# Optimization experiments

Hardware: AMD Instinct MI355X
Metric: run time of the kernel (lower is better)

Reference implementation:

```python
import jax, jax.numpy as jnp
import numpy as np

N_ITER = 4  # n_iter
NEG = -1e9  # masked-score fill (softmax-safe stand-in for -inf)


def _mfvi(x, mask, ternary, global_):
    """MFVI message passing between head (H) and node (Z) variables with global nodes.

    x:       [B, L, D] unary scores for Z nodes
    mask:    [B, L]    padding mask (nonzero = valid token)
    ternary: [D, D, H] ternary factor scores f(Z_i=a, Z_j=b, H-channel c)
    global_: [G, D, H] global-node factor scores
    Defaults: norm=softmax, regularize=1, stepsize=1, damping=0, async_update,
    no tensor decomposition, mode='all-attn', block_msg=False, output_prob=False.
    """
    B, L, D = x.shape
    m1 = (mask != 0)                                             # [B, L]
    pair_valid = m1[:, None, :, None] & m1[:, None, None, :]     # [B, 1, L, L]
    unary = x                                                    # pos_embed='none'
    Qz = jax.nn.softmax(unary, axis=-1)                          # [B, L, D]
    F_Z = unary
    neg = jnp.asarray(NEG, x.dtype)
    for _ in range(N_ITER):
        # --- H update: scores for head variable H_{i,c} over candidate heads j ---
        # F_Hs[n,h,i,j] = sum_{a,b} Qz[n,i,a] * ternary[a,b,h] * Qz[n,j,b]
        F_Hs = jnp.einsum('nia,abh,njb->nhij', Qz, ternary, Qz)  # [B, H, L, L]
        F_Hs = jnp.where(pair_valid, F_Hs, neg)
        # global-node columns: F_Hg[n,h,i,g] = sum_a Qz[n,i,a] * global_[g,a,h]
        F_Hg = jnp.einsum('nia,gah->nhig', Qz, global_)          # [B, H, L, G]
        F_H = jnp.concatenate([F_Hs, F_Hg], axis=-1)             # [B, H, L, L+G]
        Q_H = jax.nn.softmax(F_H, axis=-1)                       # regularize_H = 1
        Qhs, Qhg = Q_H[..., :L], Q_H[..., L:]
        # --- Z update (async: uses fresh Q_H) ---
        # message to Z_i from its chosen head j
        msg_i = jnp.einsum('nhij,njb,abh->nia', Qhs, Qz, ternary)
        # message to Z_j from dependents i (block_msg=False keeps it)
        msg_j = jnp.einsum('nhij,nia,abh->njb', Qhs, Qz, ternary)
        # message to Z_i from global nodes
        msg_g = jnp.einsum('nhig,gah->nia', Qhg, global_)
        F_Z = unary + msg_i + msg_j + msg_g                      # [B, L, D]
        Qz = jax.nn.softmax(F_Z, axis=-1)                        # regularize_Z = 1
    # output_prob=False -> unnormalized scores, zeroed at padding
    return jnp.where(m1[..., None], F_Z, jnp.zeros_like(F_Z))


def setup_inputs() -> dict:
    key = jax.random.key(0)
    k1, k2, k3 = jax.random.split(key, 3)
    B, L, D, H, G = 4, 1024, 128, 8, 64
    x = jax.random.normal(k1, (B, L, D), dtype=jnp.float32)
    mask = jnp.ones((B, L), dtype=jnp.int32)
    ternary = jax.random.normal(k2, (D, D, H), dtype=jnp.float32)          # init std=1
    global_ = jax.random.normal(k3, (G, D, H), dtype=jnp.float32) / np.sqrt(D)
    return {"x": x, "mask": mask, "ternary": ternary, "global_": global_}


def reference(x, mask, ternary, global_):
    return _mfvi(x, mask, ternary, global_)
```

## Files before the change

### kernel.cpp

```cpp
#include <hip/hip_runtime.h>
#include <math.h>

#define Bn 4
#define Ln 1024
#define Dn 128
#define Hn 8
#define Gn 64
#define NITERS 4

typedef _Float16 f16;
typedef _Float16 half8 __attribute__((ext_vector_type(8)));
typedef _Float16 half4v __attribute__((ext_vector_type(4)));
typedef float floatx4 __attribute__((ext_vector_type(4)));

#define WPAD 136
#define PPAD 72

#define MFMA(a, b, c) __builtin_amdgcn_mfma_f32_16x16x32_f16((a), (b), (c), 0, 0, 0)

__device__ __forceinline__ void gl_lds16(const f16* g, f16* l) {
    __builtin_amdgcn_global_load_lds(
        (const __attribute__((address_space(1))) void*)(g),
        (__attribute__((address_space(3))) void*)(l),
        16, 0, 0);
}

__device__ __forceinline__ void issue_tiles(const f16* us, const f16* ub, int sb,
                                            f16* UsB, f16* UbB, int w, int l) {
    #pragma unroll
    for (int k = 0; k < 4; k++) {
        int c = w * 4 + k;
        {
            int r = c * 4 + (l >> 4); int g = (l & 15) ^ (r & 7);
            gl_lds16(us + (size_t)r * Dn + g * 8, UsB + c * 512);
        }
        {
            int r = c * 8 + (l >> 3); int g = (l & 7) ^ (r & 7);
            gl_lds16(ub + (size_t)r * sb + g * 8, UbB + c * 512);
        }
    }
}

__global__ void repack_kernel(const float* __restrict__ ter, const float* __restrict__ glb,
                              f16* __restrict__ TpA, f16* __restrict__ TpB,
                              f16* __restrict__ GpA, f16* __restrict__ Gpt) {
    int idx = blockIdx.x * 256 + threadIdx.x;
    if (idx < Dn * Dn * Hn) {
        int h = idx % Hn; int b = (idx / Hn) % Dn; int a = idx / (Hn * Dn);
        f16 v = (f16)ter[idx];
        TpA[((size_t)h * Dn + a) * Dn + b] = v;
        TpB[((size_t)h * Dn + b) * Dn + a] = v;
    }
    if (idx < Gn * Dn * Hn) {
        int h = idx % Hn; int a = (idx / Hn) % Dn; int g = idx / (Hn * Dn);
        f16 v = (f16)glb[idx];
        GpA[((size_t)h * Gn + g) * Dn + a] = v;
        Gpt[((size_t)h * Dn + a) * Gn + g] = v;
    }
}

__global__ void softmax_rows_kernel(const float* __restrict__ in, f16* __restrict__ out) {
    int row = blockIdx.x;
    int t = threadIdx.x;
    __shared__ float red[2];
    float v = in[(size_t)row * Dn + t];
    float m = v;
    #pragma unroll
    for (int off = 1; off < 64; off <<= 1) m = fmaxf(m, __shfl_xor(m, off, 64));
    if ((t & 63) == 0) red[t >> 6] = m;
    __syncthreads();
    m = fmaxf(red[0], red[1]);
    float e = __expf(v - m);
    float s = e;
    #pragma unroll
    for (int off = 1; off < 64; off <<= 1) s += __shfl_xor(s, off, 64);
    __syncthreads();
    if ((t & 63) == 0) red[t >> 6] = s;
    __syncthreads();
    s = red[0] + red[1];
    out[(size_t)row * Dn + t] = (f16)(e / s);
}

__launch_bounds__(256, 4)
__global__ void uv_kernel(const f16* __restrict__ Qz, const f16* __restrict__ TpA,
                          const f16* __restrict__ TpB,
                          f16* __restrict__ U, f16* __restrict__ Ut, f16* __restrict__ Vt) {
    int bx = blockIdx.x;
    int h  = blockIdx.y;
    int n  = blockIdx.z;
    int t  = threadIdx.x;
    int w = t >> 6, l = t & 63, m = l & 15, q = l >> 4;

    __shared__ __align__(16) f16 Ts[128 * WPAD];

    int jrow = bx * 64 + w * 16 + m;
    const f16* qbase = Qz + ((size_t)n * Ln + jrow) * Dn;
    half8 aq[4];
    #pragma unroll
    for (int ks = 0; ks < 4; ks++)
        aq[ks] = *(const half8*)(qbase + ks * 32 + q * 8);

    size_t hoff = (size_t)(n * Hn + h);
    int jr0 = bx * 64 + w * 16 + 4 * q;

    {
        const f16* src = TpA + (size_t)h * Dn * Dn;
        for (int ii = 0; ii < 8; ii++) {
            int idx = t + 256 * ii; int r = idx >> 4, c = idx & 15;
            *(float4*)&Ts[r * WPAD + c * 8] = *(const float4*)(src + (size_t)r * Dn + c * 8);
        }
        __syncthreads();
        #pragma unroll
        for (int ct = 0; ct < 8; ct++) {
            floatx4 acc = {0.f, 0.f, 0.f, 0.f};
            #pragma unroll
            for (int ks = 0; ks < 4; ks++) {
                half8 b = *(const half8*)&Ts[(ct * 16 + m) * WPAD + ks * 32 + q * 8];
                acc = MFMA(aq[ks], b, acc);
            }
            f16* ub = U + (hoff * Ln + jr0) * Dn + ct * 16 + m;
            #pragma unroll
            for (int reg = 0; reg < 4; reg++) ub[(size_t)reg * Dn] = (f16)acc[reg];
            half4v pk = { (f16)acc[0], (f16)acc[1], (f16)acc[2], (f16)acc[3] };
            *(half4v*)(Ut + (hoff * Dn + ct * 16 + m) * Ln + jr0) = pk;
        }
        __syncthreads();
    }
    {
        const f16* src = TpB + (size_t)h * Dn * Dn;
        for (int ii = 0; ii < 8; ii++) {
            int idx = t + 256 * ii; int r = idx >> 4, c = idx & 15;
            *(float4*)&Ts[r * WPAD + c * 8] = *(const float4*)(src + (size_t)r * Dn + c * 8);
        }
        __syncthreads();
        #pragma unroll
        for (int ct = 0; ct < 8; ct++) {
            floatx4 acc = {0.f, 0.f, 0.f, 0.f};
            #pragma unroll
            for (int ks = 0; ks < 4; ks++) {
                half8 b = *(const half8*)&Ts[(ct * 16 + m) * WPAD + ks * 32 + q * 8];
                acc = MFMA(aq[ks], b, acc);
            }
            half4v pk = { (f16)acc[0], (f16)acc[1], (f16)acc[2], (f16)acc[3] };
            *(half4v*)(Vt + (hoff * Dn + ct * 16 + m) * Ln + jr0) = pk;
        }
    }
}

__launch_bounds__(256, 2)
__global__ void msgi_kernel(const f16* __restrict__ Qz, const f16* __restrict__ U,
                            const f16* __restrict__ Ut, const f16* __restrict__ GpA,
                            const f16* __restrict__ Gpt, const int* __restrict__ mask,
                            f16* __restrict__ Macc, float* __restrict__ rowLinv) {
    int p = blockIdx.x;
    int h  = p & 7;
    int it = (p >> 3) & 15;
    int n  = p >> 7;
    int t = threadIdx.x;
    int w = t >> 6, l = t & 63, m = l & 15, q = l >> 4;
    int rh = w >> 1, ch = w & 1;
    int ih = w >> 1, ah = w & 1;

    __shared__ __align__(16) f16 Us[2][64 * 128];
    __shared__ __align__(16) f16 Ub[2][128 * 64];
    __shared__ __align__(16) f16 Ps[64 * PPAD];
    __shared__ int jms[2][64];
    __shared__ float lpart[2][64];
    __shared__ float linvS[64];

    half8 bq[2][4];
    #pragma unroll
    for (int ib = 0; ib < 2; ib++) {
        const f16* qr = Qz + ((size_t)n * Ln + it * 64 + ch * 32 + ib * 16 + m) * Dn;
        #pragma unroll
        for (int ks = 0; ks < 4; ks++)
            bq[ib][ks] = *(const half8*)(qr + ks * 32 + q * 8);
    }
    int im[2];
    #pragma unroll
    for (int ib = 0; ib < 2; ib++)
        im[ib] = mask[n * Ln + it * 64 + ch * 32 + ib * 16 + m];

    float lacc[2] = {0.f, 0.f};
    floatx4 Oacc[2][4];
    #pragma unroll
    for (int ib = 0; ib < 2; ib++)
        #pragma unroll
        for (int at = 0; at < 4; at++) Oacc[ib][at] = (floatx4){0.f, 0.f, 0.f, 0.f};

    size_t hoff = (size_t)(n * Hn + h);

    issue_tiles(U + hoff * Ln * Dn, Ut + hoff * Dn * Ln, Ln, Us[0], Ub[0], w, l);
    if (t < 64) jms[0][t] = mask[n * Ln + t];
    __syncthreads();

    for (int jt = 0; jt < 17; jt++) {
        int cur = jt & 1, nxt = cur ^ 1;
        if (jt + 1 < 17) {
            const f16 *us, *ub; int sb;
            if (jt + 1 < 16) {
                us = U + (hoff * Ln + (size_t)(jt + 1) * 64) * Dn;
                ub = Ut + hoff * Dn * Ln + (jt + 1) * 64;
                sb = Ln;
            } else {
                us = GpA + (size_t)h * Gn * Dn;
                ub = Gpt + (size_t)h * Dn * Gn;
                sb = Gn;
            }
            issue_tiles(us, ub, sb, Us[nxt], Ub[nxt], w, l);
            if (t < 64) jms[nxt][t] = (jt + 1 < 16) ? mask[n * Ln + (jt + 1) * 64 + t] : 1;
        }
        int isg = (jt == 16);
        #pragma unroll
        for (int jb = 0; jb < 2; jb++) {
            int r0 = rh * 32 + jb * 16 + m;
            half8 au[4];
            #pragma unroll
            for (int ks = 0; ks < 4; ks++)
                au[ks] = *(const half8*)&Us[cur][((size_t)r0 << 7) + ((((ks << 2) + q)) ^ (r0 & 7)) * 8];
            int jmr[4];
            #pragma unroll
            for (int reg = 0; reg < 4; reg++)
                jmr[reg] = jms[cur][rh * 32 + jb * 16 + 4 * q + reg];
            #pragma unroll
            for (int ib = 0; ib < 2; ib++) {
                floatx4 s = {0.f, 0.f, 0.f, 0.f};
                #pragma unroll
                for (int ks = 0; ks < 4; ks++) s = MFMA(au[ks], bq[ib][ks], s);
                half4v pk;
                #pragma unroll
                for (int reg = 0; reg < 4; reg++) {
                    float p2 = (isg || (im[ib] && jmr[reg])) ? __expf(fminf(s[reg], 11.f)) : 0.f;
                    lacc[ib] += p2;
                    pk[reg] = (f16)p2;
                }
                *(half4v*)&Ps[(ch * 32 + ib * 16 + m) * PPAD + rh * 32 + jb * 16 + 4 * q] = pk;
            }
        }
        __syncthreads();

        #pragma unroll
        for (int kst = 0; kst < 2; kst++) {
            half8 aP[2];
            #pragma unroll
            for (int ib = 0; ib < 2; ib++)
                aP[ib] = *(const half8*)&Ps[(ih * 32 + ib * 16 + m) * PPAD + kst * 32 + q * 8];
            #pragma unroll
            for (int at = 0; at < 4; at++) {
                int r0 = ah * 64 + at * 16 + m;
                half8 bU = *(const half8*)&Ub[cur][((size_t)r0 << 6) + ((((kst << 2) + q)) ^ (r0 & 7)) * 8];
                #pragma unroll
                for (int ib = 0; ib < 2; ib++)
                    Oacc[ib][at] = MFMA(aP[ib], bU, Oacc[ib][at]);
            }
        }
        __syncthreads();
    }

    #pragma unroll
    for (int ib = 0; ib < 2; ib++) {
        float v = lacc[ib];
        v += __shfl_xor(v, 16, 64);
        v += __shfl_xor(v, 32, 64);
        lacc[ib] = v;
    }
    if (q == 0) {
        lpart[rh][ch * 32 + m] = lacc[0];
        lpart[rh][ch * 32 + 16 + m] = lacc[1];
    }
    __syncthreads();
    size_t rbase = hoff * Ln + (size_t)it * 64;
    if (t < 64) {
        float inv = 1.0f / (lpart[0][t] + lpart[1][t]);
        linvS[t] = inv;
        int mk = mask[n * Ln + it * 64 + t];
        rowLinv[rbase + t] = mk ? inv : 0.f;
    }
    __syncthreads();
    f16* Mo = Macc + rbase * Dn;
    #pragma unroll
    for (int ib = 0; ib < 2; ib++)
        #pragma unroll
        for (int reg = 0; reg < 4; reg++) {
            int row = ih * 32 + ib * 16 + 4 * q + reg;
            float inv = linvS[row];
            #pragma unroll
            for (int at = 0; at < 4; at++)
                Mo[(size_t)row * Dn + ah * 64 + at * 16 + m] = (f16)(Oacc[ib][at][reg] * inv);
        }
}

__launch_bounds__(256, 2)
__global__ void msgj_kernel(const f16* __restrict__ Qz, const f16* __restrict__ U,
                            const f16* __restrict__ Vt, const int* __restrict__ mask,
                            const float* __restrict__ rowLinv, f16* __restrict__ Macc) {
    int p = blockIdx.x;
    int h  = p & 7;
    int jt = (p >> 3) & 15;
    int n  = p >> 7;
    int t = threadIdx.x;
    int w = t >> 6, l = t & 63, m = l & 15, q = l >> 4;
    int ihs = w >> 1, jhs = w & 1;
    int jh2 = w >> 1, bh = w & 1;

    __shared__ __align__(16) f16 Qs[2][64 * 128];
    __shared__ __align__(16) f16 Vb[2][128 * 64];
    __shared__ __align__(16) f16 Psj[64 * PPAD];
    __shared__ float lvS[2][64];

    size_t hoff = (size_t)(n * Hn + h);

    half8 bu[2][4];
    #pragma unroll
    for (int jb = 0; jb < 2; jb++) {
        const f16* ur = U + (hoff * Ln + (size_t)jt * 64 + jhs * 32 + jb * 16 + m) * Dn;
        #pragma unroll
        for (int ks = 0; ks < 4; ks++)
            bu[jb][ks] = *(const half8*)(ur + ks * 32 + q * 8);
    }
    int jm[2];
    #pragma unroll
    for (int jb = 0; jb < 2; jb++)
        jm[jb] = mask[n * Ln + jt * 64 + jhs * 32 + jb * 16 + m];

    floatx4 Oacc[2][4];
    #pragma unroll
    for (int jb = 0; jb < 2; jb++)
        #pragma unroll
        for (int bt = 0; bt < 4; bt++) Oacc[jb][bt] = (floatx4){0.f, 0.f, 0.f, 0.f};

    issue_tiles(Qz + (size_t)n * Ln * Dn, Vt + hoff * Dn * Ln, Ln, Qs[0], Vb[0], w, l);
    if (t < 64) lvS[0][t] = rowLinv[hoff * Ln + t];
    __syncthreads();

    for (int it2 = 0; it2 < 16; it2++) {
        int cur = it2 & 1, nxt = cur ^ 1;
        if (it2 + 1 < 16) {
            issue_tiles(Qz + ((size_t)n * Ln + (size_t)(it2 + 1) * 64) * Dn,
                        Vt + hoff * Dn * Ln + (it2 + 1) * 64, Ln, Qs[nxt], Vb[nxt], w, l);
            if (t < 64) lvS[nxt][t] = rowLinv[hoff * Ln + (it2 + 1) * 64 + t];
        }
        #pragma unroll
        for (int ib = 0; ib < 2; ib++) {
            int r0 = ihs * 32 + ib * 16 + m;
            half8 aq2[4];
            #pragma unroll
            for (int ks = 0; ks < 4; ks++)
                aq2[ks] = *(const half8*)&Qs[cur][((size_t)r0 << 7) + ((((ks << 2) + q)) ^ (r0 & 7)) * 8];
            float lv[4];
            #pragma unroll
            for (int reg = 0; reg < 4; reg++)
                lv[reg] = lvS[cur][ihs * 32 + ib * 16 + 4 * q + reg];
            #pragma unroll
            for (int jb = 0; jb < 2; jb++) {
                floatx4 s = {0.f, 0.f, 0.f, 0.f};
                #pragma unroll
                for (int ks = 0; ks < 4; ks++) s = MFMA(aq2[ks], bu[jb][ks], s);
                half4v pk;
                #pragma unroll
                for (int reg = 0; reg < 4; reg++) {
                    float p2 = jm[jb] ? __expf(fminf(s[reg], 11.f)) * lv[reg] : 0.f;
                    pk[reg] = (f16)p2;
                }
                *(half4v*)&Psj[(jhs * 32 + jb * 16 + m) * PPAD + ihs * 32 + ib * 16 + 4 * q] = pk;
            }
        }
        __syncthreads();

        #pragma unroll
        for (int kst = 0; kst < 2; kst++) {
            half8 aP[2];
            #pragma unroll
            for (int jb = 0; jb < 2; jb++)
                aP[jb] = *(const half8*)&Psj[(jh2 * 32 + jb * 16 + m) * PPAD + kst * 32 + q * 8];
            #pragma unroll
            for (int bt = 0; bt < 4; bt++) {
                int r0 = bh * 64 + bt * 16 + m;
                half8 bV = *(const half8*)&Vb[cur][((size_t)r0 << 6) + ((((kst << 2) + q)) ^ (r0 & 7)) * 8];
                #pragma unroll
                for (int jb = 0; jb < 2; jb++)
                    Oacc[jb][bt] = MFMA(aP[jb], bV, Oacc[jb][bt]);
            }
        }
        __syncthreads();
    }

    f16* Mo = Macc + (hoff * Ln + (size_t)jt * 64) * Dn;
    #pragma unroll
    for (int jb = 0; jb < 2; jb++)
        #pragma unroll
        for (int reg = 0; reg < 4; reg++) {
            int row = jh2 * 32 + jb * 16 + 4 * q + reg;
            #pragma unroll
            for (int bt = 0; bt < 4; bt++) {
                f16* p2 = &Mo[(size_t)row * Dn + bh * 64 + bt * 16 + m];
                *p2 = (f16)((float)*p2 + Oacc[jb][bt][reg]);
            }
        }
}

__global__ void combine_kernel(const float* __restrict__ x, const f16* __restrict__ Macc,
                               const int* __restrict__ mask, float* __restrict__ out,
                               f16* __restrict__ Qzh, int do_softmax, int do_mask) {
    int row = blockIdx.x;
    int t = threadIdx.x;
    __shared__ float red[2];
    int n = row >> 10;
    float acc = x[(size_t)row * Dn + t];
    const f16* mp = Macc + (size_t)n * Hn * Ln * Dn + (size_t)(row & 1023) * Dn + t;
    #pragma unroll
    for (int h = 0; h < Hn; h++) acc += (float)mp[(size_t)h * Ln * Dn];
    float o = acc;
    if (do_mask && mask[row] == 0) o = 0.f;
    out[(size_t)row * Dn + t] = o;
    if (do_softmax) {
        float m = acc;
        #pragma unroll
        for (int off = 1; off < 64; off <<= 1) m = fmaxf(m, __shfl_xor(m, off, 64));
        if ((t & 63) == 0) red[t >> 6] = m;
        __syncthreads();
        m = fmaxf(red[0], red[1]);
        float e = __expf(acc - m);
        float s = e;
        #pragma unroll
        for (int off = 1; off < 64; off <<= 1) s += __shfl_xor(s, off, 64);
        __syncthreads();
        if ((t & 63) == 0) red[t >> 6] = s;
        __syncthreads();
        s = red[0] + red[1];
        Qzh[(size_t)row * Dn + t] = (f16)(e / s);
    }
}

extern "C" void kernel_launch(void* const* d_in, const int* in_sizes, int n_in,
                              void* d_out, int out_size, void* d_ws, size_t ws_size,
                              hipStream_t stream) {
    const float* x       = (const float*)d_in[0];
    const int*   mask    = (const int*)d_in[1];
    const float* ternary = (const float*)d_in[2];
    const float* global_ = (const float*)d_in[3];
    float* out = (float*)d_out;
    (void)ws_size; (void)n_in; (void)in_sizes; (void)out_size;

    char* ws = (char*)d_ws;
    size_t o = 0;
    f16* Qzh = (f16*)(ws + o); o += (size_t)Bn * Ln * Dn * 2;
    f16* U   = (f16*)(ws + o); o += (size_t)Bn * Hn * Ln * Dn * 2;
    f16* Ut  = (f16*)(ws + o); o += (size_t)Bn * Hn * Ln * Dn * 2;
    f16* Vt  = (f16*)(ws + o); o += (size_t)Bn * Hn * Ln * Dn * 2;
    f16* TpA = (f16*)(ws + o); o += (size_t)Hn * Dn * Dn * 2;
    f16* TpB = (f16*)(ws + o); o += (size_t)Hn * Dn * Dn * 2;
    f16* GpA = (f16*)(ws + o); o += (size_t)Hn * Gn * Dn * 2;
    f16* Gpt = (f16*)(ws + o); o += (size_t)Hn * Dn * Gn * 2;
    float* rowLinv = (float*)(ws + o); o += (size_t)Bn * Hn * Ln * 4;
    f16* Macc = (f16*)(ws + o); o += (size_t)Bn * Hn * Ln * Dn * 2;

    repack_kernel<<<(Dn * Dn * Hn + 255) / 256, 256, 0, stream>>>(ternary, global_, TpA, TpB, GpA, Gpt);
    softmax_rows_kernel<<<Bn * Ln, 128, 0, stream>>>(x, Qzh);

    for (int it = 0; it < NITERS; it++) {
        uv_kernel<<<dim3(Ln / 64, Hn, Bn), 256, 0, stream>>>(Qzh, TpA, TpB, U, Ut, Vt);
        msgi_kernel<<<dim3(Ln / 64 * Hn * Bn), 256, 0, stream>>>(Qzh, U, Ut, GpA, Gpt, mask, Macc, rowLinv);
        msgj_kernel<<<dim3(Ln / 64 * Hn * Bn), 256, 0, stream>>>(Qzh, U, Vt, mask, rowLinv, Macc);
        combine_kernel<<<Bn * Ln, 128, 0, stream>>>(x, Macc, mask, out, Qzh,
                                                    (it < NITERS - 1) ? 1 : 0,
                                                    (it == NITERS - 1) ? 1 : 0);
    }
}
```

Measured before the change: 384.0 us.

## Keep attention probabilities in registers by permuting Ut/Vt/Gpt column layout

Each wave now computes scores for all 64 key rows of its query half, so the MFMA output fragments can be reassembled directly into the A-operand of the next MFMA without staging P through shared memory. To make the register fragment ordering match the K dimension, the Ut, Vt and Gpt buffers are written with a permuted column order. This removes the Ps/Psj LDS round trip and one barrier per tile, and the row-sum reduction no longer needs cross-wave partials. In exchange, the score MFMAs are duplicated across the two waves that share a query half, which doubles that part of the work.

```diff
diff --git a/kernel.cpp b/kernel.cpp
--- a/kernel.cpp
+++ b/kernel.cpp
@@ -14,9 +14,10 @@
 typedef float floatx4 __attribute__((ext_vector_type(4)));
 
 #define WPAD 136
-#define PPAD 72
 
 #define MFMA(a, b, c) __builtin_amdgcn_mfma_f32_16x16x32_f16((a), (b), (c), 0, 0, 0)
+
+union h8u { half8 h; half4v v[2]; };
 
 __device__ __forceinline__ void gl_lds16(const f16* g, f16* l) {
     __builtin_amdgcn_global_load_lds(
@@ -55,7 +56,8 @@
         int h = idx % Hn; int a = (idx / Hn) % Dn; int g = idx / (Hn * Dn);
         f16 v = (f16)glb[idx];
         GpA[((size_t)h * Gn + g) * Dn + a] = v;
-        Gpt[((size_t)h * Dn + a) * Gn + g] = v;
+        int pos = ((g >> 5) << 5) | (((g >> 2) & 3) << 3) | (((g >> 4) & 1) << 2) | (g & 3);
+        Gpt[((size_t)h * Dn + a) * Gn + pos] = v;
     }
 }
 
@@ -102,6 +104,7 @@
 
     size_t hoff = (size_t)(n * Hn + h);
     int jr0 = bx * 64 + w * 16 + 4 * q;
+    int jrp = bx * 64 + (w >> 1) * 32 + q * 8 + (w & 1) * 4;
 
     {
         const f16* src = TpA + (size_t)h * Dn * Dn;
@@ -122,7 +125,7 @@
             #pragma unroll
             for (int reg = 0; reg < 4; reg++) ub[(size_t)reg * Dn] = (f16)acc[reg];
             half4v pk = { (f16)acc[0], (f16)acc[1], (f16)acc[2], (f16)acc[3] };
-            *(half4v*)(Ut + (hoff * Dn + ct * 16 + m) * Ln + jr0) = pk;
+            *(half4v*)(Ut + (hoff * Dn + ct * 16 + m) * Ln + jrp) = pk;
         }
         __syncthreads();
     }
@@ -142,7 +145,7 @@
                 acc = MFMA(aq[ks], b, acc);
             }
             half4v pk = { (f16)acc[0], (f16)acc[1], (f16)acc[2], (f16)acc[3] };
-            *(half4v*)(Vt + (hoff * Dn + ct * 16 + m) * Ln + jr0) = pk;
+            *(half4v*)(Vt + (hoff * Dn + ct * 16 + m) * Ln + jrp) = pk;
         }
     }
 }
@@ -158,14 +161,12 @@
     int n  = p >> 7;
     int t = threadIdx.x;
     int w = t >> 6, l = t & 63, m = l & 15, q = l >> 4;
-    int rh = w >> 1, ch = w & 1;
-    int ih = w >> 1, ah = w & 1;
+    int ch = w & 1;
+    int ah = w >> 1;
 
     __shared__ __align__(16) f16 Us[2][64 * 128];
     __shared__ __align__(16) f16 Ub[2][128 * 64];
-    __shared__ __align__(16) f16 Ps[64 * PPAD];
-    __shared__ int jms[2][64];
-    __shared__ float lpart[2][64];
+    __shared__ __align__(16) int jms[2][64];
     __shared__ float linvS[64];
 
     half8 bq[2][4];
@@ -211,17 +212,16 @@
             if (t < 64) jms[nxt][t] = (jt + 1 < 16) ? mask[n * Ln + (jt + 1) * 64 + t] : 1;
         }
         int isg = (jt == 16);
-        #pragma unroll
-        for (int jb = 0; jb < 2; jb++) {
-            int r0 = rh * 32 + jb * 16 + m;
+        half4v hv[4][2];
+        #pragma unroll
+        for (int jb = 0; jb < 4; jb++) {
+            int r0 = jb * 16 + m;
             half8 au[4];
             #pragma unroll
             for (int ks = 0; ks < 4; ks++)
                 au[ks] = *(const half8*)&Us[cur][((size_t)r0 << 7) + ((((ks << 2) + q)) ^ (r0 & 7)) * 8];
-            int jmr[4];
-            #pragma unroll
-            for (int reg = 0; reg < 4; reg++)
-                jmr[reg] = jms[cur][rh * 32 + jb * 16 + 4 * q + reg];
+            int4 jmr = *(const int4*)&jms[cur][jb * 16 + 4 * q];
+            int jm4[4] = { jmr.x, jmr.y, jmr.z, jmr.w };
             #pragma unroll
             for (int ib = 0; ib < 2; ib++) {
                 floatx4 s = {0.f, 0.f, 0.f, 0.f};
@@ -230,21 +230,24 @@
                 half4v pk;
                 #pragma unroll
                 for (int reg = 0; reg < 4; reg++) {
-                    float p2 = (isg || (im[ib] && jmr[reg])) ? __expf(fminf(s[reg], 11.f)) : 0.f;
+                    float p2 = (isg || (im[ib] && jm4[reg])) ? __expf(fminf(s[reg], 11.f)) : 0.f;
                     lacc[ib] += p2;
                     pk[reg] = (f16)p2;
                 }
-                *(half4v*)&Ps[(ch * 32 + ib * 16 + m) * PPAD + rh * 32 + jb * 16 + 4 * q] = pk;
-            }
-        }
-        __syncthreads();
+                hv[jb][ib] = pk;
+            }
+        }
 
         #pragma unroll
         for (int kst = 0; kst < 2; kst++) {
             half8 aP[2];
             #pragma unroll
-            for (int ib = 0; ib < 2; ib++)
-                aP[ib] = *(const half8*)&Ps[(ih * 32 + ib * 16 + m) * PPAD + kst * 32 + q * 8];
+            for (int ib = 0; ib < 2; ib++) {
+                h8u u;
+                u.v[0] = hv[2 * kst][ib];
+                u.v[1] = hv[2 * kst + 1][ib];
+                aP[ib] = u.h;
+            }
             #pragma unroll
             for (int at = 0; at < 4; at++) {
                 int r0 = ah * 64 + at * 16 + m;
@@ -264,25 +267,23 @@
         v += __shfl_xor(v, 32, 64);
         lacc[ib] = v;
     }
-    if (q == 0) {
-        lpart[rh][ch * 32 + m] = lacc[0];
-        lpart[rh][ch * 32 + 16 + m] = lacc[1];
+    if (ah == 0 && q == 0) {
+        linvS[ch * 32 + m]      = 1.0f / lacc[0];
+        linvS[ch * 32 + 16 + m] = 1.0f / lacc[1];
     }
     __syncthreads();
     size_t rbase = hoff * Ln + (size_t)it * 64;
     if (t < 64) {
-        float inv = 1.0f / (lpart[0][t] + lpart[1][t]);
-        linvS[t] = inv;
+        float inv = linvS[t];
         int mk = mask[n * Ln + it * 64 + t];
         rowLinv[rbase + t] = mk ? inv : 0.f;
     }
-    __syncthreads();
     f16* Mo = Macc + rbase * Dn;
     #pragma unroll
     for (int ib = 0; ib < 2; ib++)
         #pragma unroll
         for (int reg = 0; reg < 4; reg++) {
-            int row = ih * 32 + ib * 16 + 4 * q + reg;
+            int row = ch * 32 + ib * 16 + 4 * q + reg;
             float inv = linvS[row];
             #pragma unroll
             for (int at = 0; at < 4; at++)
@@ -300,13 +301,12 @@
     int n  = p >> 7;
     int t = threadIdx.x;
     int w = t >> 6, l = t & 63, m = l & 15, q = l >> 4;
-    int ihs = w >> 1, jhs = w & 1;
-    int jh2 = w >> 1, bh = w & 1;
+    int jhs = w & 1;
+    int bh  = w >> 1;
 
     __shared__ __align__(16) f16 Qs[2][64 * 128];
     __shared__ __align__(16) f16 Vb[2][128 * 64];
-    __shared__ __align__(16) f16 Psj[64 * PPAD];
-    __shared__ float lvS[2][64];
+    __shared__ __align__(16) float lvS[2][64];
 
     size_t hoff = (size_t)(n * Hn + h);
 
@@ -340,17 +340,16 @@
                         Vt + hoff * Dn * Ln + (it2 + 1) * 64, Ln, Qs[nxt], Vb[nxt], w, l);
             if (t < 64) lvS[nxt][t] = rowLinv[hoff * Ln + (it2 + 1) * 64 + t];
         }
-        #pragma unroll
-        for (int ib = 0; ib < 2; ib++) {
-            int r0 = ihs * 32 + ib * 16 + m;
+        half4v hv[4][2];
+        #pragma unroll
+        for (int ibt = 0; ibt < 4; ibt++) {
+            int r0 = ibt * 16 + m;
             half8 aq2[4];
             #pragma unroll
             for (int ks = 0; ks < 4; ks++)
                 aq2[ks] = *(const half8*)&Qs[cur][((size_t)r0 << 7) + ((((ks << 2) + q)) ^ (r0 & 7)) * 8];
-            float lv[4];
-            #pragma unroll
-            for (int reg = 0; reg < 4; reg++)
-                lv[reg] = lvS[cur][ihs * 32 + ib * 16 + 4 * q + reg];
+            float4 lv = *(const float4*)&lvS[cur][ibt * 16 + 4 * q];
+            float lv4[4] = { lv.x, lv.y, lv.z, lv.w };
             #pragma unroll
             for (int jb = 0; jb < 2; jb++) {
                 floatx4 s = {0.f, 0.f, 0.f, 0.f};
@@ -359,20 +358,23 @@
                 half4v pk;
                 #pragma unroll
                 for (int reg = 0; reg < 4; reg++) {
-                    float p2 = jm[jb] ? __expf(fminf(s[reg], 11.f)) * lv[reg] : 0.f;
+                    float p2 = jm[jb] ? __expf(fminf(s[reg], 11.f)) * lv4[reg] : 0.f;
                     pk[reg] = (f16)p2;
                 }
-                *(half4v*)&Psj[(jhs * 32 + jb * 16 + m) * PPAD + ihs * 32 + ib * 16 + 4 * q] = pk;
-            }
-        }
-        __syncthreads();
+                hv[ibt][jb] = pk;
+            }
+        }
 
         #pragma unroll
         for (int kst = 0; kst < 2; kst++) {
             half8 aP[2];
             #pragma unroll
-            for (int jb = 0; jb < 2; jb++)
-                aP[jb] = *(const half8*)&Psj[(jh2 * 32 + jb * 16 + m) * PPAD + kst * 32 + q * 8];
+            for (int jb = 0; jb < 2; jb++) {
+                h8u u;
+                u.v[0] = hv[2 * kst][jb];
+                u.v[1] = hv[2 * kst + 1][jb];
+                aP[jb] = u.h;
+            }
             #pragma unroll
             for (int bt = 0; bt < 4; bt++) {
                 int r0 = bh * 64 + bt * 16 + m;
@@ -390,7 +392,7 @@
     for (int jb = 0; jb < 2; jb++)
         #pragma unroll
         for (int reg = 0; reg < 4; reg++) {
-            int row = jh2 * 32 + jb * 16 + 4 * q + reg;
+            int row = jhs * 32 + jb * 16 + 4 * q + reg;
             #pragma unroll
             for (int bt = 0; bt < 4; bt++) {
                 f16* p2 = &Mo[(size_t)row * Dn + bh * 64 + bt * 16 + m];
```

New measurement: 453.1 us. 18.0% more time.

## Keep attention probabilities in registers via 16x16x16 MFMA and split-K across eight waves

Applied to the files above, without the earlier changes.

msgi and msgj now run 512-thread blocks in which each wave computes a 16-row slice of the score tile. Each wave feeds its exp'd probabilities straight from the accumulator registers into 16x16x16 MFMAs, so the LDS P-buffer round trip and the barrier between the two GEMMs are gone. The four K-slices are then reduced through LDS at the end. Padding masking moves into uv_kernel as a -64 bias on U rows, which drops per-element mask checks, but masking now relies on exp saturation rather than exact zeros. The tradeoffs are more accumulator registers, a multi-stage LDS reduction at the end, and a different occupancy profile.

```diff
diff --git a/kernel.cpp b/kernel.cpp
--- a/kernel.cpp
+++ b/kernel.cpp
@@ -14,9 +14,9 @@
 typedef float floatx4 __attribute__((ext_vector_type(4)));
 
 #define WPAD 136
-#define PPAD 72
-
-#define MFMA(a, b, c) __builtin_amdgcn_mfma_f32_16x16x32_f16((a), (b), (c), 0, 0, 0)
+
+#define MFMA(a, b, c)   __builtin_amdgcn_mfma_f32_16x16x32_f16((a), (b), (c), 0, 0, 0)
+#define MFMA16(a, b, c) __builtin_amdgcn_mfma_f32_16x16x16f16((a), (b), (c), 0, 0, 0)
 
 __device__ __forceinline__ void gl_lds16(const f16* g, f16* l) {
     __builtin_amdgcn_global_load_lds(
@@ -25,11 +25,11 @@
         16, 0, 0);
 }
 
-__device__ __forceinline__ void issue_tiles(const f16* us, const f16* ub, int sb,
-                                            f16* UsB, f16* UbB, int w, int l) {
-    #pragma unroll
-    for (int k = 0; k < 4; k++) {
-        int c = w * 4 + k;
+__device__ __forceinline__ void issue_tiles8(const f16* us, const f16* ub, int sb,
+                                             f16* UsB, f16* UbB, int w, int l) {
+    #pragma unroll
+    for (int k = 0; k < 2; k++) {
+        int c = w * 2 + k;
         {
             int r = c * 4 + (l >> 4); int g = (l & 15) ^ (r & 7);
             gl_lds16(us + (size_t)r * Dn + g * 8, UsB + c * 512);
@@ -83,7 +83,7 @@
 
 __launch_bounds__(256, 4)
 __global__ void uv_kernel(const f16* __restrict__ Qz, const f16* __restrict__ TpA,
-                          const f16* __restrict__ TpB,
+                          const f16* __restrict__ TpB, const int* __restrict__ mask,
                           f16* __restrict__ U, f16* __restrict__ Ut, f16* __restrict__ Vt) {
     int bx = blockIdx.x;
     int h  = blockIdx.y;
@@ -103,6 +103,11 @@
     size_t hoff = (size_t)(n * Hn + h);
     int jr0 = bx * 64 + w * 16 + 4 * q;
 
+    float bias[4];
+    #pragma unroll
+    for (int reg = 0; reg < 4; reg++)
+        bias[reg] = mask[n * Ln + jr0 + reg] ? 0.f : -64.f;
+
     {
         const f16* src = TpA + (size_t)h * Dn * Dn;
         for (int ii = 0; ii < 8; ii++) {
@@ -119,9 +124,13 @@
                 acc = MFMA(aq[ks], b, acc);
             }
             f16* ub = U + (hoff * Ln + jr0) * Dn + ct * 16 + m;
+            half4v pk;
             #pragma unroll
-            for (int reg = 0; reg < 4; reg++) ub[(size_t)reg * Dn] = (f16)acc[reg];
-            half4v pk = { (f16)acc[0], (f16)acc[1], (f16)acc[2], (f16)acc[3] };
+            for (int reg = 0; reg < 4; reg++) {
+                f16 v = (f16)(acc[reg] + bias[reg]);
+                ub[(size_t)reg * Dn] = v;
+                pk[reg] = v;
+            }
             *(half4v*)(Ut + (hoff * Dn + ct * 16 + m) * Ln + jr0) = pk;
         }
         __syncthreads();
@@ -147,7 +156,7 @@
     }
 }
 
-__launch_bounds__(256, 2)
+__launch_bounds__(512, 4)
 __global__ void msgi_kernel(const f16* __restrict__ Qz, const f16* __restrict__ U,
                             const f16* __restrict__ Ut, const f16* __restrict__ GpA,
                             const f16* __restrict__ Gpt, const int* __restrict__ mask,
@@ -158,42 +167,36 @@
     int n  = p >> 7;
     int t = threadIdx.x;
     int w = t >> 6, l = t & 63, m = l & 15, q = l >> 4;
-    int rh = w >> 1, ch = w & 1;
-    int ih = w >> 1, ah = w & 1;
+    int ih2 = w >> 2;
+    int kq  = w & 3;
 
     __shared__ __align__(16) f16 Us[2][64 * 128];
     __shared__ __align__(16) f16 Ub[2][128 * 64];
-    __shared__ __align__(16) f16 Ps[64 * PPAD];
-    __shared__ int jms[2][64];
-    __shared__ float lpart[2][64];
+    __shared__ float lredS[4][64];
     __shared__ float linvS[64];
 
     half8 bq[2][4];
     #pragma unroll
     for (int ib = 0; ib < 2; ib++) {
-        const f16* qr = Qz + ((size_t)n * Ln + it * 64 + ch * 32 + ib * 16 + m) * Dn;
+        const f16* qr = Qz + ((size_t)n * Ln + it * 64 + ih2 * 32 + ib * 16 + m) * Dn;
         #pragma unroll
         for (int ks = 0; ks < 4; ks++)
             bq[ib][ks] = *(const half8*)(qr + ks * 32 + q * 8);
     }
-    int im[2];
+
+    float lacc[2] = {0.f, 0.f};
+    floatx4 Oacc[2][8];
     #pragma unroll
     for (int ib = 0; ib < 2; ib++)
-        im[ib] = mask[n * Ln + it * 64 + ch * 32 + ib * 16 + m];
-
-    float lacc[2] = {0.f, 0.f};
-    floatx4 Oacc[2][4];
-    #pragma unroll
-    for (int ib = 0; ib < 2; ib++)
-        #pragma unroll
-        for (int at = 0; at < 4; at++) Oacc[ib][at] = (floatx4){0.f, 0.f, 0.f, 0.f};
+        #pragma unroll
+        for (int at = 0; at < 8; at++) Oacc[ib][at] = (floatx4){0.f, 0.f, 0.f, 0.f};
 
     size_t hoff = (size_t)(n * Hn + h);
 
-    issue_tiles(U + hoff * Ln * Dn, Ut + hoff * Dn * Ln, Ln, Us[0], Ub[0], w, l);
-    if (t < 64) jms[0][t] = mask[n * Ln + t];
-    __syncthreads();
-
+    issue_tiles8(U + hoff * Ln * Dn, Ut + hoff * Dn * Ln, Ln, Us[0], Ub[0], w, l);
+    __syncthreads();
+
+    int r0 = kq * 16 + m;
     for (int jt = 0; jt < 17; jt++) {
         int cur = jt & 1, nxt = cur ^ 1;
         if (jt + 1 < 17) {
@@ -207,52 +210,30 @@
                 ub = Gpt + (size_t)h * Dn * Gn;
                 sb = Gn;
             }
-            issue_tiles(us, ub, sb, Us[nxt], Ub[nxt], w, l);
-            if (t < 64) jms[nxt][t] = (jt + 1 < 16) ? mask[n * Ln + (jt + 1) * 64 + t] : 1;
-        }
-        int isg = (jt == 16);
-        #pragma unroll
-        for (int jb = 0; jb < 2; jb++) {
-            int r0 = rh * 32 + jb * 16 + m;
-            half8 au[4];
-            #pragma unroll
-            for (int ks = 0; ks < 4; ks++)
-                au[ks] = *(const half8*)&Us[cur][((size_t)r0 << 7) + ((((ks << 2) + q)) ^ (r0 & 7)) * 8];
-            int jmr[4];
-            #pragma unroll
-            for (int reg = 0; reg < 4; reg++)
-                jmr[reg] = jms[cur][rh * 32 + jb * 16 + 4 * q + reg];
-            #pragma unroll
-            for (int ib = 0; ib < 2; ib++) {
-                floatx4 s = {0.f, 0.f, 0.f, 0.f};
-                #pragma unroll
-                for (int ks = 0; ks < 4; ks++) s = MFMA(au[ks], bq[ib][ks], s);
-                half4v pk;
-                #pragma unroll
-                for (int reg = 0; reg < 4; reg++) {
-                    float p2 = (isg || (im[ib] && jmr[reg])) ? __expf(fminf(s[reg], 11.f)) : 0.f;
-                    lacc[ib] += p2;
-                    pk[reg] = (f16)p2;
-                }
-                *(half4v*)&Ps[(ch * 32 + ib * 16 + m) * PPAD + rh * 32 + jb * 16 + 4 * q] = pk;
-            }
-        }
-        __syncthreads();
-
-        #pragma unroll
-        for (int kst = 0; kst < 2; kst++) {
-            half8 aP[2];
-            #pragma unroll
-            for (int ib = 0; ib < 2; ib++)
-                aP[ib] = *(const half8*)&Ps[(ih * 32 + ib * 16 + m) * PPAD + kst * 32 + q * 8];
-            #pragma unroll
-            for (int at = 0; at < 4; at++) {
-                int r0 = ah * 64 + at * 16 + m;
-                half8 bU = *(const half8*)&Ub[cur][((size_t)r0 << 6) + ((((kst << 2) + q)) ^ (r0 & 7)) * 8];
-                #pragma unroll
-                for (int ib = 0; ib < 2; ib++)
-                    Oacc[ib][at] = MFMA(aP[ib], bU, Oacc[ib][at]);
-            }
+            issue_tiles8(us, ub, sb, Us[nxt], Ub[nxt], w, l);
+        }
+        floatx4 s0 = {0.f, 0.f, 0.f, 0.f}, s1 = {0.f, 0.f, 0.f, 0.f};
+        #pragma unroll
+        for (int ks = 0; ks < 4; ks++) {
+            half8 au = *(const half8*)&Us[cur][((size_t)r0 << 7) + ((((ks << 2) + q)) ^ (r0 & 7)) * 8];
+            s0 = MFMA(au, bq[0][ks], s0);
+            s1 = MFMA(au, bq[1][ks], s1);
+        }
+        half4v hv0, hv1;
+        #pragma unroll
+        for (int reg = 0; reg < 4; reg++) {
+            float p0 = __expf(fminf(s0[reg], 11.f));
+            float p1 = __expf(fminf(s1[reg], 11.f));
+            lacc[0] += p0; lacc[1] += p1;
+            hv0[reg] = (f16)p0; hv1[reg] = (f16)p1;
+        }
+        #pragma unroll
+        for (int at = 0; at < 8; at++) {
+            int ra = at * 16 + m;
+            half4v bU = *(const half4v*)&Ub[cur][((size_t)ra << 6) +
+                          ((((kq << 1) + (q >> 1)) ^ (ra & 7)) << 3) + ((q & 1) << 2)];
+            Oacc[0][at] = MFMA16(hv0, bU, Oacc[0][at]);
+            Oacc[1][at] = MFMA16(hv1, bU, Oacc[1][at]);
         }
         __syncthreads();
     }
@@ -265,32 +246,57 @@
         lacc[ib] = v;
     }
     if (q == 0) {
-        lpart[rh][ch * 32 + m] = lacc[0];
-        lpart[rh][ch * 32 + 16 + m] = lacc[1];
+        lredS[kq][ih2 * 32 + m]      = lacc[0];
+        lredS[kq][ih2 * 32 + 16 + m] = lacc[1];
     }
     __syncthreads();
     size_t rbase = hoff * Ln + (size_t)it * 64;
     if (t < 64) {
-        float inv = 1.0f / (lpart[0][t] + lpart[1][t]);
+        float inv = 1.0f / (lredS[0][t] + lredS[1][t] + lredS[2][t] + lredS[3][t]);
         linvS[t] = inv;
-        int mk = mask[n * Ln + it * 64 + t];
-        rowLinv[rbase + t] = mk ? inv : 0.f;
-    }
-    __syncthreads();
-    f16* Mo = Macc + rbase * Dn;
-    #pragma unroll
-    for (int ib = 0; ib < 2; ib++)
-        #pragma unroll
-        for (int reg = 0; reg < 4; reg++) {
-            int row = ih * 32 + ib * 16 + 4 * q + reg;
-            float inv = linvS[row];
+        rowLinv[rbase + t] = mask[n * Ln + it * 64 + t] ? inv : 0.f;
+    }
+    if (kq >= 2) {
+        float* ox = (kq == 2 ? (float*)Us : (float*)Ub) + (size_t)ih2 * 4096;
+        #pragma unroll
+        for (int c = 0; c < 16; c++)
+            *(floatx4*)&ox[(size_t)c * 256 + l * 4] = Oacc[c >> 3][c & 7];
+    }
+    __syncthreads();
+    if (kq < 2) {
+        const float* ox = (kq == 0 ? (const float*)Us : (const float*)Ub) + (size_t)ih2 * 4096;
+        #pragma unroll
+        for (int c = 0; c < 16; c++)
+            Oacc[c >> 3][c & 7] += *(const floatx4*)&ox[(size_t)c * 256 + l * 4];
+    }
+    __syncthreads();
+    if (kq == 1) {
+        float* ox = (float*)Us + (size_t)ih2 * 4096;
+        #pragma unroll
+        for (int c = 0; c < 16; c++)
+            *(floatx4*)&ox[(size_t)c * 256 + l * 4] = Oacc[c >> 3][c & 7];
+    }
+    __syncthreads();
+    if (kq == 0) {
+        const float* ox = (const float*)Us + (size_t)ih2 * 4096;
+        f16* Mo = Macc + rbase * Dn;
+        #pragma unroll
+        for (int c = 0; c < 16; c++)
+            Oacc[c >> 3][c & 7] += *(const floatx4*)&ox[(size_t)c * 256 + l * 4];
+        #pragma unroll
+        for (int ib = 0; ib < 2; ib++)
             #pragma unroll
-            for (int at = 0; at < 4; at++)
-                Mo[(size_t)row * Dn + ah * 64 + at * 16 + m] = (f16)(Oacc[ib][at][reg] * inv);
-        }
-}
-
-__launch_bounds__(256, 2)
+            for (int reg = 0; reg < 4; reg++) {
+                int row = ih2 * 32 + ib * 16 + 4 * q + reg;
+                float inv = linvS[row];
+                #pragma unroll
+                for (int at = 0; at < 8; at++)
+                    Mo[(size_t)row * Dn + at * 16 + m] = (f16)(Oacc[ib][at][reg] * inv);
+            }
+    }
+}
+
+__launch_bounds__(512, 4)
 __global__ void msgj_kernel(const f16* __restrict__ Qz, const f16* __restrict__ U,
                             const f16* __restrict__ Vt, const int* __restrict__ mask,
                             const float* __restrict__ rowLinv, f16* __restrict__ Macc) {
@@ -300,103 +306,107 @@
     int n  = p >> 7;
     int t = threadIdx.x;
     int w = t >> 6, l = t & 63, m = l & 15, q = l >> 4;
-    int ihs = w >> 1, jhs = w & 1;
-    int jh2 = w >> 1, bh = w & 1;
+    int jh2 = w >> 2;
+    int iq  = w & 3;
 
     __shared__ __align__(16) f16 Qs[2][64 * 128];
     __shared__ __align__(16) f16 Vb[2][128 * 64];
-    __shared__ __align__(16) f16 Psj[64 * PPAD];
-    __shared__ float lvS[2][64];
+    __shared__ __align__(16) float lvS[2][64];
 
     size_t hoff = (size_t)(n * Hn + h);
 
     half8 bu[2][4];
     #pragma unroll
     for (int jb = 0; jb < 2; jb++) {
-        const f16* ur = U + (hoff * Ln + (size_t)jt * 64 + jhs * 32 + jb * 16 + m) * Dn;
+        const f16* ur = U + (hoff * Ln + (size_t)jt * 64 + jh2 * 32 + jb * 16 + m) * Dn;
         #pragma unroll
         for (int ks = 0; ks < 4; ks++)
             bu[jb][ks] = *(const half8*)(ur + ks * 32 + q * 8);
     }
-    int jm[2];
+
+    floatx4 Oacc[2][8];
     #pragma unroll
     for (int jb = 0; jb < 2; jb++)
-        jm[jb] = mask[n * Ln + jt * 64 + jhs * 32 + jb * 16 + m];
-
-    floatx4 Oacc[2][4];
-    #pragma unroll
-    for (int jb = 0; jb < 2; jb++)
-        #pragma unroll
-        for (int bt = 0; bt < 4; bt++) Oacc[jb][bt] = (floatx4){0.f, 0.f, 0.f, 0.f};
-
-    issue_tiles(Qz + (size_t)n * Ln * Dn, Vt + hoff * Dn * Ln, Ln, Qs[0], Vb[0], w, l);
+        #pragma unroll
+        for (int bt = 0; bt < 8; bt++) Oacc[jb][bt] = (floatx4){0.f, 0.f, 0.f, 0.f};
+
+    issue_tiles8(Qz + (size_t)n * Ln * Dn, Vt + hoff * Dn * Ln, Ln, Qs[0], Vb[0], w, l);
     if (t < 64) lvS[0][t] = rowLinv[hoff * Ln + t];
     __syncthreads();
 
+    int r0 = iq * 16 + m;
     for (int it2 = 0; it2 < 16; it2++) {
         int cur = it2 & 1, nxt = cur ^ 1;
         if (it2 + 1 < 16) {
-            issue_tiles(Qz + ((size_t)n * Ln + (size_t)(it2 + 1) * 64) * Dn,
-                        Vt + hoff * Dn * Ln + (it2 + 1) * 64, Ln, Qs[nxt], Vb[nxt], w, l);
+            issue_tiles8(Qz + ((size_t)n * Ln + (size_t)(it2 + 1) * 64) * Dn,
+                         Vt + hoff * Dn * Ln + (it2 + 1) * 64, Ln, Qs[nxt], Vb[nxt], w, l);
             if (t < 64) lvS[nxt][t] = rowLinv[hoff * Ln + (it2 + 1) * 64 + t];
         }
-        #pragma unroll
-        for (int ib = 0; ib < 2; ib++) {
-            int r0 = ihs * 32 + ib * 16 + m;
-            half8 aq2[4];
+        floatx4 s0 = {0.f, 0.f, 0.f, 0.f}, s1 = {0.f, 0.f, 0.f, 0.f};
+        #pragma unroll
+        for (int ks = 0; ks < 4; ks++) {
+            half8 aq2 = *(const half8*)&Qs[cur][((size_t)r0 << 7) + ((((ks << 2) + q)) ^ (r0 & 7)) * 8];
+            s0 = MFMA(aq2, bu[0][ks], s0);
+            s1 = MFMA(aq2, bu[1][ks], s1);
+        }
+        float4 lv = *(const float4*)&lvS[cur][iq * 16 + 4 * q];
+        float lv4[4] = { lv.x, lv.y, lv.z, lv.w };
+        half4v hv0, hv1;
+        #pragma unroll
+        for (int reg = 0; reg < 4; reg++) {
+            hv0[reg] = (f16)(__expf(fminf(s0[reg], 11.f)) * lv4[reg]);
+            hv1[reg] = (f16)(__expf(fminf(s1[reg], 11.f)) * lv4[reg]);
+        }
+        #pragma unroll
+        for (int bt = 0; bt < 8; bt++) {
+            int ra = bt * 16 + m;
+            half4v bV = *(const half4v*)&Vb[cur][((size_t)ra << 6) +
+                          ((((iq << 1) + (q >> 1)) ^ (ra & 7)) << 3) + ((q & 1) << 2)];
+            Oacc[0][bt] = MFMA16(hv0, bV, Oacc[0][bt]);
+            Oacc[1][bt] = MFMA16(hv1, bV, Oacc[1][bt]);
+        }
+        __syncthreads();
+    }
+
+    if (iq >= 2) {
+        float* ox = (iq == 2 ? (float*)Qs : (float*)Vb) + (size_t)jh2 * 4096;
+        #pragma unroll
+        for (int c = 0; c < 16; c++)
+            *(floatx4*)&ox[(size_t)c * 256 + l * 4] = Oacc[c >> 3][c & 7];
+    }
+    __syncthreads();
+    if (iq < 2) {
+        const float* ox = (iq == 0 ? (const float*)Qs : (const float*)Vb) + (size_t)jh2 * 4096;
+        #pragma unroll
+        for (int c = 0; c < 16; c++)
+            Oacc[c >> 3][c & 7] += *(const floatx4*)&ox[(size_t)c * 256 + l * 4];
+    }
+    __syncthreads();
+    if (iq == 1) {
+        float* ox = (float*)Qs + (size_t)jh2 * 4096;
+        #pragma unroll
+        for (int c = 0; c < 16; c++)
+            *(floatx4*)&ox[(size_t)c * 256 + l * 4] = Oacc[c >> 3][c & 7];
+    }
+    __syncthreads();
+    if (iq == 0) {
+        const float* ox = (const float*)Qs + (size_t)jh2 * 4096;
+        #pragma unroll
+        for (int c = 0; c < 16; c++)
+            Oacc[c >> 3][c & 7] += *(const floatx4*)&ox[(size_t)c * 256 + l * 4];
+        f16* Mo = Macc + (hoff * Ln + (size_t)jt * 64) * Dn;
+        #pragma unroll
+        for (int jb = 0; jb < 2; jb++)
             #pragma unroll
-            for (int ks = 0; ks < 4; ks++)
-                aq2[ks] = *(const half8*)&Qs[cur][((size_t)r0 << 7) + ((((ks << 2) + q)) ^ (r0 & 7)) * 8];
-            float lv[4];
-            #pragma unroll
-            for (int reg = 0; reg < 4; reg++)
-                lv[reg] = lvS[cur][ihs * 32 + ib * 16 + 4 * q + reg];
-            #pragma unroll
-            for (int jb = 0; jb < 2; jb++) {
-                floatx4 s = {0.f, 0.f, 0.f, 0.f};
+            for (int reg = 0; reg < 4; reg++) {
+                int row = jh2 * 32 + jb * 16 + 4 * q + reg;
                 #pragma unroll
-                for (int ks = 0; ks < 4; ks++) s = MFMA(aq2[ks], bu[jb][ks], s);
-                half4v pk;
-                #pragma unroll
-                for (int reg = 0; reg < 4; reg++) {
-                    float p2 = jm[jb] ? __expf(fminf(s[reg], 11.f)) * lv[reg] : 0.f;
-                    pk[reg] = (f16)p2;
+                for (int bt = 0; bt < 8; bt++) {
+                    f16* p2 = &Mo[(size_t)row * Dn + bt * 16 + m];
+                    *p2 = (f16)((float)*p2 + Oacc[jb][bt][reg]);
                 }
-                *(half4v*)&Psj[(jhs * 32 + jb * 16 + m) * PPAD + ihs * 32 + ib * 16 + 4 * q] = pk;
-            }
-        }
-        __syncthreads();
-
-        #pragma unroll
-        for (int kst = 0; kst < 2; kst++) {
-            half8 aP[2];
-            #pragma unroll
-            for (int jb = 0; jb < 2; jb++)
-                aP[jb] = *(const half8*)&Psj[(jh2 * 32 + jb * 16 + m) * PPAD + kst * 32 + q * 8];
-            #pragma unroll
-            for (int bt = 0; bt < 4; bt++) {
-                int r0 = bh * 64 + bt * 16 + m;
-                half8 bV = *(const half8*)&Vb[cur][((size_t)r0 << 6) + ((((kst << 2) + q)) ^ (r0 & 7)) * 8];
-                #pragma unroll
-                for (int jb = 0; jb < 2; jb++)
-                    Oacc[jb][bt] = MFMA(aP[jb], bV, Oacc[jb][bt]);
-            }
-        }
-        __syncthreads();
-    }
-
-    f16* Mo = Macc + (hoff * Ln + (size_t)jt * 64) * Dn;
-    #pragma unroll
-    for (int jb = 0; jb < 2; jb++)
-        #pragma unroll
-        for (int reg = 0; reg < 4; reg++) {
-            int row = jh2 * 32 + jb * 16 + 4 * q + reg;
-            #pragma unroll
-            for (int bt = 0; bt < 4; bt++) {
-                f16* p2 = &Mo[(size_t)row * Dn + bh * 64 + bt * 16 + m];
-                *p2 = (f16)((float)*p2 + Oacc[jb][bt][reg]);
-            }
-        }
+            }
+    }
 }
 
 __global__ void combine_kernel(const float* __restrict__ x, const f16* __restrict__ Macc,
@@ -459,9 +469,9 @@
     softmax_rows_kernel<<<Bn * Ln, 128, 0, stream>>>(x, Qzh);
 
     for (int it = 0; it < NITERS; it++) {
-        uv_kernel<<<dim3(Ln / 64, Hn, Bn), 256, 0, stream>>>(Qzh, TpA, TpB, U, Ut, Vt);
-        msgi_kernel<<<dim3(Ln / 64 * Hn * Bn), 256, 0, stream>>>(Qzh, U, Ut, GpA, Gpt, mask, Macc, rowLinv);
-        msgj_kernel<<<dim3(Ln / 64 * Hn * Bn), 256, 0, stream>>>(Qzh, U, Vt, mask, rowLinv, Macc);
+        uv_kernel<<<dim3(Ln / 64, Hn, Bn), 256, 0, stream>>>(Qzh, TpA, TpB, mask, U, Ut, Vt);
+        msgi_kernel<<<dim3(Ln / 64 * Hn * Bn), 512, 0, stream>>>(Qzh, U, Ut, GpA, Gpt, mask, Macc, rowLinv);
+        msgj_kernel<<<dim3(Ln / 64 * Hn * Bn), 512, 0, stream>>>(Qzh, U, Vt, mask, rowLinv, Macc);
         combine_kernel<<<Bn * Ln, 128, 0, stream>>>(x, Macc, mask, out, Qzh,
                                                     (it < NITERS - 1) ? 1 : 0,
                                                     (it == NITERS - 1) ? 1 : 0);
```

New measurement: 473.4 us. +23.3%, slower.
